# Kernel tuning notes

Measured on AMD Instinct MI355X. Metric: run time of the kernel, lower is better.

Reference implementation:

```python
import jax, jax.numpy as jnp
import numpy as np

INPUT_SIZE = 128
OUTPUT_SIZE = 128
HIDDEN = 8
BATCH = 1024
N = INPUT_SIZE * OUTPUT_SIZE  # number of tiny subnetworks


def setup_inputs() -> dict:
    key = jax.random.key(0)
    ks = jax.random.split(key, 7)
    s = 0.5  # modest init scale
    return {
        "x": jax.random.normal(ks[0], (BATCH, INPUT_SIZE), dtype=jnp.float32),
        "W1": jax.random.normal(ks[1], (N, HIDDEN, 1), dtype=jnp.float32) * s,
        "b1": jax.random.normal(ks[2], (N, HIDDEN), dtype=jnp.float32) * s,
        "W2": jax.random.normal(ks[3], (N, HIDDEN, HIDDEN), dtype=jnp.float32) * s,
        "b2": jax.random.normal(ks[4], (N, HIDDEN), dtype=jnp.float32) * s,
        "W3": jax.random.normal(ks[5], (N, 1, HIDDEN), dtype=jnp.float32) * s,
        "b3": jax.random.normal(ks[6], (N, 1), dtype=jnp.float32) * s,
    }


def reference(x, W1, b1, W2, b2, W3, b3):
    # x: [B, input_size]. Subnet n = i*output_size + o consumes feature i.
    B = x.shape[0]
    # x.T repeat_interleave(output_size, dim=0).unsqueeze(-1) -> [N, B, 1]
    xe = jnp.repeat(x.T, OUTPUT_SIZE, axis=0)[:, :, None]
    # torch Linear: y = x @ W.T + b, batched over subnet dim n
    h = jax.nn.relu(jnp.einsum('nbi,nhi->nbh', xe, W1) + b1[:, None, :])
    h = jax.nn.relu(jnp.einsum('nbi,nhi->nbh', h, W2) + b2[:, None, :])
    o = jnp.einsum('nbh,noh->nbo', h, W3) + b3[:, None, :]  # [N, B, 1]
    o = o[..., 0].reshape(INPUT_SIZE, OUTPUT_SIZE, B)
    return o.sum(axis=0).T  # [B, output_size]
```

## Files before the change

kernel.cpp:

```cpp
#include <hip/hip_runtime.h>

#define INPUT_SIZE 128
#define OUTPUT_SIZE 128
#define HIDDEN 8
#define BATCH 1024

#define ICH 16
#define IPC (INPUT_SIZE / ICH)
#define TPB 128
#define BPT 8
#define WPI 100

__global__ void transpose_x_kernel(const float* __restrict__ x,
                                   float* __restrict__ xT) {
    __shared__ float tile[32][33];
    const int i0 = blockIdx.x * 32;
    const int b0 = blockIdx.y * 32;
    const int tx = threadIdx.x;
    const int ty = threadIdx.y;
#pragma unroll
    for (int r = ty; r < 32; r += 8)
        tile[r][tx] = x[(b0 + r) * INPUT_SIZE + (i0 + tx)];
    __syncthreads();
#pragma unroll
    for (int r = ty; r < 32; r += 8)
        xT[(i0 + r) * BATCH + (b0 + tx)] = tile[tx][r];
}

__global__ void zero_out_kernel(float* __restrict__ out, int n) {
    int idx = blockIdx.x * blockDim.x + threadIdx.x;
    if (idx < n) out[idx] = 0.0f;
}

template <bool PARTIALS>
__global__ __launch_bounds__(TPB, 2)
void mlpkan_kernel(const float* __restrict__ xT,
                   const float* __restrict__ W1, const float* __restrict__ b1,
                   const float* __restrict__ W2, const float* __restrict__ b2,
                   const float* __restrict__ W3, const float* __restrict__ b3,
                   float* __restrict__ partials, float* __restrict__ out) {
    __shared__ float wlds[IPC][WPI];

    const int o   = blockIdx.x;
    const int ic  = blockIdx.y;
    const int tid = threadIdx.x;

    {
        const int ii  = tid >> 4;
        const int idx = tid & 15;
        const int n   = (ic * IPC + ii) * OUTPUT_SIZE + o;
        const float4 v = *(const float4*)(W2 + (size_t)n * 64 + idx * 4);
        *(float4*)&wlds[ii][16 + idx * 4] = v;

        if (tid < 64) {
            const int ii2 = tid >> 3;
            const int k   = tid & 7;
            const int n2  = (ic * IPC + ii2) * OUTPUT_SIZE + o;
            wlds[ii2][0  + k] = W1[(size_t)n2 * HIDDEN + k];
            wlds[ii2][8  + k] = b1[(size_t)n2 * HIDDEN + k];
            wlds[ii2][80 + k] = b2[(size_t)n2 * HIDDEN + k];
            wlds[ii2][88 + k] = W3[(size_t)n2 * HIDDEN + k];
            if (k == 0) wlds[ii2][96] = b3[n2];
        }
    }
    __syncthreads();

    float acc[BPT];
#pragma unroll
    for (int j = 0; j < BPT; ++j) acc[j] = 0.0f;

    for (int ii = 0; ii < IPC; ++ii) {
        const int i = ic * IPC + ii;

        float s[BPT];
#pragma unroll
        for (int j = 0; j < BPT; ++j)
            s[j] = xT[(size_t)i * BATCH + tid + j * TPB];

        const float4* wq = (const float4*)(&wlds[ii][0]);
        const float4 w1a = wq[0],  w1b = wq[1];
        const float4 b1a = wq[2],  b1b = wq[3];
        float4 w2q[16];
#pragma unroll
        for (int q = 0; q < 16; ++q) w2q[q] = wq[4 + q];
        const float4 b2a = wq[20], b2b = wq[21];
        const float4 w3a = wq[22], w3b = wq[23];
        const float  b3r = wlds[ii][96];

        const float w1r[8] = {w1a.x, w1a.y, w1a.z, w1a.w, w1b.x, w1b.y, w1b.z, w1b.w};
        const float b1r[8] = {b1a.x, b1a.y, b1a.z, b1a.w, b1b.x, b1b.y, b1b.z, b1b.w};
        const float b2r[8] = {b2a.x, b2a.y, b2a.z, b2a.w, b2b.x, b2b.y, b2b.z, b2b.w};
        const float w3r[8] = {w3a.x, w3a.y, w3a.z, w3a.w, w3b.x, w3b.y, w3b.z, w3b.w};

#pragma unroll
        for (int j = 0; j < BPT; ++j) {
            const float sj = s[j];
            float h1[8];
#pragma unroll
            for (int k = 0; k < 8; ++k)
                h1[k] = fmaxf(fmaf(w1r[k], sj, b1r[k]), 0.0f);
            float h2[8];
#pragma unroll
            for (int h = 0; h < 8; ++h) {
                const float4 qa = w2q[2 * h];
                const float4 qb = w2q[2 * h + 1];
                float v = b2r[h];
                v = fmaf(qa.x, h1[0], v); v = fmaf(qa.y, h1[1], v);
                v = fmaf(qa.z, h1[2], v); v = fmaf(qa.w, h1[3], v);
                v = fmaf(qb.x, h1[4], v); v = fmaf(qb.y, h1[5], v);
                v = fmaf(qb.z, h1[6], v); v = fmaf(qb.w, h1[7], v);
                h2[h] = fmaxf(v, 0.0f);
            }
            float v = b3r;
#pragma unroll
            for (int k = 0; k < 8; ++k)
                v = fmaf(w3r[k], h2[k], v);
            acc[j] += v;
        }
    }

    if (PARTIALS) {
#pragma unroll
        for (int j = 0; j < BPT; ++j)
            partials[((size_t)ic * OUTPUT_SIZE + o) * BATCH + tid + j * TPB] = acc[j];
    } else {
#pragma unroll
        for (int j = 0; j < BPT; ++j)
            atomicAdd(&out[(size_t)(tid + j * TPB) * OUTPUT_SIZE + o], acc[j]);
    }
}

__global__ void reduce_kernel(const float* __restrict__ partials,
                              float* __restrict__ out) {
    __shared__ float tile[32][33];
    const int o0 = blockIdx.x * 32;
    const int b0 = blockIdx.y * 32;
    const int tx = threadIdx.x;
    const int ty = threadIdx.y;
#pragma unroll
    for (int r = ty; r < 32; r += 8) {
        float v = 0.0f;
#pragma unroll
        for (int ic = 0; ic < ICH; ++ic)
            v += partials[((size_t)ic * OUTPUT_SIZE + o0 + r) * BATCH + b0 + tx];
        tile[r][tx] = v;
    }
    __syncthreads();
#pragma unroll
    for (int r = ty; r < 32; r += 8)
        out[(size_t)(b0 + r) * OUTPUT_SIZE + o0 + tx] = tile[tx][r];
}

extern "C" void kernel_launch(void* const* d_in, const int* in_sizes, int n_in,
                              void* d_out, int out_size, void* d_ws, size_t ws_size,
                              hipStream_t stream) {
    const float* x  = (const float*)d_in[0];
    const float* W1 = (const float*)d_in[1];
    const float* b1 = (const float*)d_in[2];
    const float* W2 = (const float*)d_in[3];
    const float* b2 = (const float*)d_in[4];
    const float* W3 = (const float*)d_in[5];
    const float* b3 = (const float*)d_in[6];
    float* out = (float*)d_out;

    const size_t xt_elems   = (size_t)INPUT_SIZE * BATCH;
    const size_t part_elems = (size_t)ICH * OUTPUT_SIZE * BATCH;
    const size_t need_bytes = (xt_elems + part_elems) * sizeof(float);

    dim3 tgrid(INPUT_SIZE / 32, BATCH / 32);
    dim3 tblk(32, 8);
    dim3 mgrid(OUTPUT_SIZE, ICH);

    if (ws_size >= need_bytes) {
        float* xT       = (float*)d_ws;
        float* partials = xT + xt_elems;
        transpose_x_kernel<<<tgrid, tblk, 0, stream>>>(x, xT);
        mlpkan_kernel<true><<<mgrid, TPB, 0, stream>>>(xT, W1, b1, W2, b2, W3, b3,
                                                       partials, out);
        dim3 rgrid(OUTPUT_SIZE / 32, BATCH / 32);
        reduce_kernel<<<rgrid, tblk, 0, stream>>>(partials, out);
    } else if (ws_size >= xt_elems * sizeof(float)) {
        float* xT = (float*)d_ws;
        transpose_x_kernel<<<tgrid, tblk, 0, stream>>>(x, xT);
        const int n = BATCH * OUTPUT_SIZE;
        zero_out_kernel<<<(n + 255) / 256, 256, 0, stream>>>(out, n);
        mlpkan_kernel<false><<<mgrid, TPB, 0, stream>>>(xT, W1, b1, W2, b2, W3, b3,
                                                        nullptr, out);
    } else {
        const int n = BATCH * OUTPUT_SIZE;
        zero_out_kernel<<<(n + 255) / 256, 256, 0, stream>>>(out, n);
        mlpkan_kernel<false><<<mgrid, TPB, 0, stream>>>(x, W1, b1, W2, b2, W3, b3,
                                                        nullptr, out);
    }
}
```

Baseline: 110.8 us.

## Convert W2 to fp16 and use packed fdot2 for the hidden layer

A fused prep kernel now transposes x and converts W2 to packed fp16 in the workspace. The main kernel drops the LDS weight staging and the barrier, reads per-subnet weights straight from global memory each iteration, and computes the 8x8 hidden layer with v_dot2 fp16 dot products instead of scalar FMAs. It also raises the occupancy hint to 3 and uses wider blocks in the reduce kernel. This cuts ALU work and W2 bandwidth, but lowers the precision of the hidden layer and drops the fallback path when the workspace is small.

After: 111.2 us. Within noise of the previous version (+0.4%).

```diff
diff --git a/kernel.cpp b/kernel.cpp
--- a/kernel.cpp
+++ b/kernel.cpp
@@ -9,22 +9,46 @@
 #define IPC (INPUT_SIZE / ICH)
 #define TPB 128
 #define BPT 8
-#define WPI 100
-
-__global__ void transpose_x_kernel(const float* __restrict__ x,
-                                   float* __restrict__ xT) {
-    __shared__ float tile[32][33];
-    const int i0 = blockIdx.x * 32;
-    const int b0 = blockIdx.y * 32;
-    const int tx = threadIdx.x;
-    const int ty = threadIdx.y;
-#pragma unroll
-    for (int r = ty; r < 32; r += 8)
-        tile[r][tx] = x[(b0 + r) * INPUT_SIZE + (i0 + tx)];
-    __syncthreads();
-#pragma unroll
-    for (int r = ty; r < 32; r += 8)
-        xT[(i0 + r) * BATCH + (b0 + tx)] = tile[tx][r];
+
+typedef __fp16 half2v __attribute__((ext_vector_type(2)));
+
+#if defined(__has_builtin)
+#if __has_builtin(__builtin_amdgcn_fdot2)
+#define HAS_FDOT2 1
+#endif
+#endif
+#ifndef HAS_FDOT2
+#define HAS_FDOT2 0
+#endif
+
+__global__ void prep_kernel(const float* __restrict__ x,
+                            const float* __restrict__ W2,
+                            float* __restrict__ xT,
+                            __fp16* __restrict__ W2h) {
+    if (blockIdx.x < 128) {
+        __shared__ float tile[32][33];
+        const int bx = blockIdx.x;
+        const int i0 = (bx & 3) * 32;
+        const int b0 = (bx >> 2) * 32;
+        const int tx = threadIdx.x & 31;
+        const int ty = threadIdx.x >> 5;
+#pragma unroll
+        for (int r = ty; r < 32; r += 8)
+            tile[r][tx] = x[(b0 + r) * INPUT_SIZE + (i0 + tx)];
+        __syncthreads();
+#pragma unroll
+        for (int r = ty; r < 32; r += 8)
+            xT[(i0 + r) * BATCH + (b0 + tx)] = tile[tx][r];
+    } else {
+        const size_t idx = (size_t)(blockIdx.x - 128) * 256 + threadIdx.x;
+        const float4 v = *(const float4*)(W2 + 4 * idx);
+        const half2v a = __builtin_amdgcn_cvt_pkrtz(v.x, v.y);
+        const half2v b = __builtin_amdgcn_cvt_pkrtz(v.z, v.w);
+        float2 st;
+        st.x = __builtin_bit_cast(float, a);
+        st.y = __builtin_bit_cast(float, b);
+        *(float2*)(W2h + 4 * idx) = st;
+    }
 }
 
 __global__ void zero_out_kernel(float* __restrict__ out, int n) {
@@ -33,59 +57,49 @@
 }
 
 template <bool PARTIALS>
-__global__ __launch_bounds__(TPB, 2)
+__global__ __launch_bounds__(TPB, 3)
 void mlpkan_kernel(const float* __restrict__ xT,
                    const float* __restrict__ W1, const float* __restrict__ b1,
-                   const float* __restrict__ W2, const float* __restrict__ b2,
+                   const __fp16* __restrict__ W2h, const float* __restrict__ b2,
                    const float* __restrict__ W3, const float* __restrict__ b3,
                    float* __restrict__ partials, float* __restrict__ out) {
-    __shared__ float wlds[IPC][WPI];
-
     const int o   = blockIdx.x;
     const int ic  = blockIdx.y;
     const int tid = threadIdx.x;
 
-    {
-        const int ii  = tid >> 4;
-        const int idx = tid & 15;
-        const int n   = (ic * IPC + ii) * OUTPUT_SIZE + o;
-        const float4 v = *(const float4*)(W2 + (size_t)n * 64 + idx * 4);
-        *(float4*)&wlds[ii][16 + idx * 4] = v;
-
-        if (tid < 64) {
-            const int ii2 = tid >> 3;
-            const int k   = tid & 7;
-            const int n2  = (ic * IPC + ii2) * OUTPUT_SIZE + o;
-            wlds[ii2][0  + k] = W1[(size_t)n2 * HIDDEN + k];
-            wlds[ii2][8  + k] = b1[(size_t)n2 * HIDDEN + k];
-            wlds[ii2][80 + k] = b2[(size_t)n2 * HIDDEN + k];
-            wlds[ii2][88 + k] = W3[(size_t)n2 * HIDDEN + k];
-            if (k == 0) wlds[ii2][96] = b3[n2];
-        }
-    }
-    __syncthreads();
-
     float acc[BPT];
 #pragma unroll
     for (int j = 0; j < BPT; ++j) acc[j] = 0.0f;
 
+#pragma unroll 1
     for (int ii = 0; ii < IPC; ++ii) {
         const int i = ic * IPC + ii;
+        const int n = i * OUTPUT_SIZE + o;
 
         float s[BPT];
 #pragma unroll
         for (int j = 0; j < BPT; ++j)
             s[j] = xT[(size_t)i * BATCH + tid + j * TPB];
 
-        const float4* wq = (const float4*)(&wlds[ii][0]);
-        const float4 w1a = wq[0],  w1b = wq[1];
-        const float4 b1a = wq[2],  b1b = wq[3];
-        float4 w2q[16];
-#pragma unroll
-        for (int q = 0; q < 16; ++q) w2q[q] = wq[4 + q];
-        const float4 b2a = wq[20], b2b = wq[21];
-        const float4 w3a = wq[22], w3b = wq[23];
-        const float  b3r = wlds[ii][96];
+        const float4 w1a = *(const float4*)(W1 + (size_t)n * 8);
+        const float4 w1b = *(const float4*)(W1 + (size_t)n * 8 + 4);
+        const float4 b1a = *(const float4*)(b1 + (size_t)n * 8);
+        const float4 b1b = *(const float4*)(b1 + (size_t)n * 8 + 4);
+        const float4 b2a = *(const float4*)(b2 + (size_t)n * 8);
+        const float4 b2b = *(const float4*)(b2 + (size_t)n * 8 + 4);
+        const float4 w3a = *(const float4*)(W3 + (size_t)n * 8);
+        const float4 w3b = *(const float4*)(W3 + (size_t)n * 8 + 4);
+        const float  bb3 = b3[n];
+
+        half2v w2p[8][4];
+#pragma unroll
+        for (int h = 0; h < 8; ++h) {
+            const float4 row = *(const float4*)((const char*)W2h + (size_t)n * 128 + h * 16);
+            w2p[h][0] = __builtin_bit_cast(half2v, row.x);
+            w2p[h][1] = __builtin_bit_cast(half2v, row.y);
+            w2p[h][2] = __builtin_bit_cast(half2v, row.z);
+            w2p[h][3] = __builtin_bit_cast(half2v, row.w);
+        }
 
         const float w1r[8] = {w1a.x, w1a.y, w1a.z, w1a.w, w1b.x, w1b.y, w1b.z, w1b.w};
         const float b1r[8] = {b1a.x, b1a.y, b1a.z, b1a.w, b1b.x, b1b.y, b1b.z, b1b.w};
@@ -99,23 +113,40 @@
 #pragma unroll
             for (int k = 0; k < 8; ++k)
                 h1[k] = fmaxf(fmaf(w1r[k], sj, b1r[k]), 0.0f);
+
+#if HAS_FDOT2
+            half2v hp[4];
+#pragma unroll
+            for (int q = 0; q < 4; ++q)
+                hp[q] = __builtin_amdgcn_cvt_pkrtz(h1[2 * q], h1[2 * q + 1]);
+
             float h2[8];
 #pragma unroll
             for (int h = 0; h < 8; ++h) {
-                const float4 qa = w2q[2 * h];
-                const float4 qb = w2q[2 * h + 1];
                 float v = b2r[h];
-                v = fmaf(qa.x, h1[0], v); v = fmaf(qa.y, h1[1], v);
-                v = fmaf(qa.z, h1[2], v); v = fmaf(qa.w, h1[3], v);
-                v = fmaf(qb.x, h1[4], v); v = fmaf(qb.y, h1[5], v);
-                v = fmaf(qb.z, h1[6], v); v = fmaf(qb.w, h1[7], v);
+#pragma unroll
+                for (int q = 0; q < 4; ++q)
+                    v = __builtin_amdgcn_fdot2(w2p[h][q], hp[q], v, false);
                 h2[h] = fmaxf(v, 0.0f);
             }
-            float v = b3r;
+#else
+            float h2[8];
+#pragma unroll
+            for (int h = 0; h < 8; ++h) {
+                float v = b2r[h];
+#pragma unroll
+                for (int q = 0; q < 4; ++q) {
+                    v = fmaf((float)w2p[h][q][0], h1[2 * q], v);
+                    v = fmaf((float)w2p[h][q][1], h1[2 * q + 1], v);
+                }
+                h2[h] = fmaxf(v, 0.0f);
+            }
+#endif
+            float v3 = bb3;
 #pragma unroll
             for (int k = 0; k < 8; ++k)
-                v = fmaf(w3r[k], h2[k], v);
-            acc[j] += v;
+                v3 = fmaf(w3r[k], h2[k], v3);
+            acc[j] += v3;
         }
     }
 
@@ -138,16 +169,16 @@
     const int tx = threadIdx.x;
     const int ty = threadIdx.y;
 #pragma unroll
-    for (int r = ty; r < 32; r += 8) {
+    for (int r = ty; r < 32; r += 16) {
         float v = 0.0f;
 #pragma unroll
-        for (int ic = 0; ic < ICH; ++ic)
-            v += partials[((size_t)ic * OUTPUT_SIZE + o0 + r) * BATCH + b0 + tx];
+        for (int icc = 0; icc < ICH; ++icc)
+            v += partials[((size_t)icc * OUTPUT_SIZE + o0 + r) * BATCH + b0 + tx];
         tile[r][tx] = v;
     }
     __syncthreads();
 #pragma unroll
-    for (int r = ty; r < 32; r += 8)
+    for (int r = ty; r < 32; r += 16)
         out[(size_t)(b0 + r) * OUTPUT_SIZE + o0 + tx] = tile[tx][r];
 }
 
@@ -165,31 +196,30 @@
 
     const size_t xt_elems   = (size_t)INPUT_SIZE * BATCH;
     const size_t part_elems = (size_t)ICH * OUTPUT_SIZE * BATCH;
-    const size_t need_bytes = (xt_elems + part_elems) * sizeof(float);
-
-    dim3 tgrid(INPUT_SIZE / 32, BATCH / 32);
-    dim3 tblk(32, 8);
+    const size_t w2h_bytes  = (size_t)16384 * 64 * sizeof(__fp16);
+    const size_t need_bytes = (xt_elems + part_elems) * sizeof(float) + w2h_bytes;
+
     dim3 mgrid(OUTPUT_SIZE, ICH);
 
     if (ws_size >= need_bytes) {
-        float* xT       = (float*)d_ws;
-        float* partials = xT + xt_elems;
-        transpose_x_kernel<<<tgrid, tblk, 0, stream>>>(x, xT);
-        mlpkan_kernel<true><<<mgrid, TPB, 0, stream>>>(xT, W1, b1, W2, b2, W3, b3,
+        float*   xT       = (float*)d_ws;
+        float*   partials = xT + xt_elems;
+        __fp16*  W2h      = (__fp16*)(partials + part_elems);
+
+        prep_kernel<<<1152, 256, 0, stream>>>(x, W2, xT, W2h);
+        mlpkan_kernel<true><<<mgrid, TPB, 0, stream>>>(xT, W1, b1, W2h, b2, W3, b3,
                                                        partials, out);
         dim3 rgrid(OUTPUT_SIZE / 32, BATCH / 32);
-        reduce_kernel<<<rgrid, tblk, 0, stream>>>(partials, out);
-    } else if (ws_size >= xt_elems * sizeof(float)) {
-        float* xT = (float*)d_ws;
-        transpose_x_kernel<<<tgrid, tblk, 0, stream>>>(x, xT);
-        const int n = BATCH * OUTPUT_SIZE;
-        zero_out_kernel<<<(n + 255) / 256, 256, 0, stream>>>(out, n);
-        mlpkan_kernel<false><<<mgrid, TPB, 0, stream>>>(xT, W1, b1, W2, b2, W3, b3,
-                                                        nullptr, out);
+        reduce_kernel<<<rgrid, dim3(32, 16), 0, stream>>>(partials, out);
     } else {
-        const int n = BATCH * OUTPUT_SIZE;
-        zero_out_kernel<<<(n + 255) / 256, 256, 0, stream>>>(out, n);
-        mlpkan_kernel<false><<<mgrid, TPB, 0, stream>>>(x, W1, b1, W2, b2, W3, b3,
-                                                        nullptr, out);
-    }
-}
+        const int nz = BATCH * OUTPUT_SIZE;
+        zero_out_kernel<<<(nz + 255) / 256, 256, 0, stream>>>(out, nz);
+        if (ws_size >= xt_elems * sizeof(float) + w2h_bytes) {
+            float*  xT  = (float*)d_ws;
+            __fp16* W2h = (__fp16*)(xT + xt_elems);
+            prep_kernel<<<1152, 256, 0, stream>>>(x, W2, xT, W2h);
+            mlpkan_kernel<false><<<mgrid, TPB, 0, stream>>>(xT, W1, b1, W2h, b2, W3, b3,
+                                                            nullptr, out);
+        }
+    }
+}
```
